# Optimization experiments

Measured on AMD Instinct MI355X. Metric: run time of the kernel, lower is better.

The kernel has to match this reference:

```python
import jax, jax.numpy as jnp
import numpy as np

C = 256

def setup_inputs() -> dict:
    key = jax.random.key(0)
    k1, k2, k3 = jax.random.split(key, 3)
    U = jax.random.normal(k1, (16, C, 128, 128), dtype=jnp.float32)
    # Conv2d 1x1 no-bias weights; kaiming-ish scale
    w_sq = jax.random.normal(k2, (C // 2, C), dtype=jnp.float32) * (1.0 / np.sqrt(C))
    w_ex = jax.random.normal(k3, (C, C // 2), dtype=jnp.float32) * (1.0 / np.sqrt(C // 2))
    return {"U": U, "w_sq": w_sq, "w_ex": w_ex}

def reference(U, w_sq, w_ex):
    # U: [B, C, H, W]
    z = jnp.mean(U, axis=(2, 3))                      # [B, C] global avg pool
    z = jnp.einsum('oc,bc->bo', w_sq, z)              # squeeze: [B, C/2]
    z = jax.nn.relu(z)
    z = jnp.einsum('oc,bc->bo', w_ex, z)              # excite: [B, C]
    s = jax.nn.sigmoid(z)                             # [B, C]
    return U * s[:, :, None, None]                    # broadcast gate over H, W
```

## Files before the change

### kernel.cpp

```cpp
#include <hip/hip_runtime.h>

#define SE_C   256
#define SE_B   16
#define SE_HW  16384

typedef float fx4 __attribute__((ext_vector_type(4)));

__global__ __launch_bounds__(256) void se_pool(const float* __restrict__ U,
                                               float* __restrict__ z) {
    const int plane = blockIdx.x;
    const fx4* Up = (const fx4*)(U + (size_t)plane * SE_HW);
    const int t = threadIdx.x;

    float sum = 0.f;
    #pragma unroll
    for (int k = 0; k < 16; ++k) {
        fx4 v = Up[t + k * 256];
        sum += (v.x + v.y) + (v.z + v.w);
    }
    #pragma unroll
    for (int off = 32; off > 0; off >>= 1)
        sum += __shfl_down(sum, off, 64);

    __shared__ float wsum[4];
    const int lane = t & 63, wid = t >> 6;
    if (lane == 0) wsum[wid] = sum;
    __syncthreads();
    if (t == 0) {
        float tot = (wsum[0] + wsum[1]) + (wsum[2] + wsum[3]);
        z[plane] = tot * (1.0f / SE_HW);
    }
}

__global__ __launch_bounds__(256) void se_fc(const float* __restrict__ z,
                                             const float* __restrict__ w_sq,
                                             const float* __restrict__ w_ex,
                                             float* __restrict__ s) {
    const int b = blockIdx.x;
    const int t = threadIdx.x;

    __shared__ float zb[SE_C];
    __shared__ float h[SE_C / 2];

    zb[t] = z[b * SE_C + t];
    __syncthreads();

    if (t < SE_C / 2) {
        const float* wr = w_sq + t * SE_C;
        float acc = 0.f;
        #pragma unroll 8
        for (int c = 0; c < SE_C; ++c) acc = fmaf(wr[c], zb[c], acc);
        h[t] = fmaxf(acc, 0.f);
    }
    __syncthreads();

    {
        const float* wr = w_ex + t * (SE_C / 2);
        float acc = 0.f;
        #pragma unroll 8
        for (int c = 0; c < SE_C / 2; ++c) acc = fmaf(wr[c], h[c], acc);
        s[b * SE_C + t] = 1.0f / (1.0f + expf(-acc));
    }
}

__global__ __launch_bounds__(256) void se_scale(const float* __restrict__ U,
                                                const float* __restrict__ s,
                                                float* __restrict__ out) {
    const int plane = blockIdx.x;
    const float g = s[plane];
    const fx4* Up = (const fx4*)(U + (size_t)plane * SE_HW);
    fx4* Op = (fx4*)(out + (size_t)plane * SE_HW);
    const int t = threadIdx.x;

    #pragma unroll
    for (int k = 0; k < 16; ++k) {
        fx4 v = Up[t + k * 256];
        v *= g;
        __builtin_nontemporal_store(v, Op + t + k * 256);
    }
}

extern "C" void kernel_launch(void* const* d_in, const int* in_sizes, int n_in,
                              void* d_out, int out_size, void* d_ws, size_t ws_size,
                              hipStream_t stream) {
    const float* U    = (const float*)d_in[0];
    const float* w_sq = (const float*)d_in[1];
    const float* w_ex = (const float*)d_in[2];
    float* out = (float*)d_out;

    float* z = (float*)d_ws;
    float* s = z + SE_B * SE_C;

    se_pool<<<SE_B * SE_C, 256, 0, stream>>>(U, z);
    se_fc<<<SE_B, 256, 0, stream>>>(z, w_sq, w_ex, s);
    se_scale<<<SE_B * SE_C, 256, 0, stream>>>(U, s, out);
}
```

Before: 135.8 us.

## Fuse SE fully-connected gate computation into scale kernel with U prefetch

```diff
diff --git a/kernel.cpp b/kernel.cpp
--- a/kernel.cpp
+++ b/kernel.cpp
@@ -32,12 +32,22 @@
     }
 }
 
-__global__ __launch_bounds__(256) void se_fc(const float* __restrict__ z,
-                                             const float* __restrict__ w_sq,
-                                             const float* __restrict__ w_ex,
-                                             float* __restrict__ s) {
-    const int b = blockIdx.x;
+__global__ __launch_bounds__(256) void se_scale_fc(const float* __restrict__ U,
+                                                   const float* __restrict__ z,
+                                                   const float* __restrict__ w_sq,
+                                                   const float* __restrict__ w_ex,
+                                                   float* __restrict__ out) {
+    const int plane = blockIdx.x;
+    const int b = plane >> 8;
+    const int c = plane & 255;
     const int t = threadIdx.x;
+
+    const fx4* Up = (const fx4*)(U + (size_t)plane * SE_HW);
+    fx4* Op = (fx4*)(out + (size_t)plane * SE_HW);
+
+    fx4 pre[8];
+    #pragma unroll
+    for (int k = 0; k < 8; ++k) pre[k] = Up[t + k * 256];
 
     __shared__ float zb[SE_C];
     __shared__ float h[SE_C / 2];
@@ -49,33 +59,25 @@
         const float* wr = w_sq + t * SE_C;
         float acc = 0.f;
         #pragma unroll 8
-        for (int c = 0; c < SE_C; ++c) acc = fmaf(wr[c], zb[c], acc);
+        for (int k = 0; k < SE_C; ++k) acc = fmaf(wr[k], zb[k], acc);
         h[t] = fmaxf(acc, 0.f);
     }
     __syncthreads();
 
-    {
-        const float* wr = w_ex + t * (SE_C / 2);
-        float acc = 0.f;
-        #pragma unroll 8
-        for (int c = 0; c < SE_C / 2; ++c) acc = fmaf(wr[c], h[c], acc);
-        s[b * SE_C + t] = 1.0f / (1.0f + expf(-acc));
-    }
-}
-
-__global__ __launch_bounds__(256) void se_scale(const float* __restrict__ U,
-                                                const float* __restrict__ s,
-                                                float* __restrict__ out) {
-    const int plane = blockIdx.x;
-    const float g = s[plane];
-    const fx4* Up = (const fx4*)(U + (size_t)plane * SE_HW);
-    fx4* Op = (fx4*)(out + (size_t)plane * SE_HW);
-    const int t = threadIdx.x;
+    const float* we = w_ex + c * (SE_C / 2);
+    float acc = 0.f;
+    #pragma unroll 8
+    for (int k = 0; k < SE_C / 2; ++k) acc = fmaf(we[k], h[k], acc);
+    const float g = 1.0f / (1.0f + __expf(-acc));
 
     #pragma unroll
-    for (int k = 0; k < 16; ++k) {
-        fx4 v = Up[t + k * 256];
-        v *= g;
+    for (int k = 0; k < 8; ++k) {
+        fx4 v = pre[k] * g;
+        __builtin_nontemporal_store(v, Op + t + k * 256);
+    }
+    #pragma unroll
+    for (int k = 8; k < 16; ++k) {
+        fx4 v = Up[t + k * 256] * g;
         __builtin_nontemporal_store(v, Op + t + k * 256);
     }
 }
@@ -89,9 +91,7 @@
     float* out = (float*)d_out;
 
     float* z = (float*)d_ws;
-    float* s = z + SE_B * SE_C;
 
     se_pool<<<SE_B * SE_C, 256, 0, stream>>>(U, z);
-    se_fc<<<SE_B, 256, 0, stream>>>(z, w_sq, w_ex, s);
-    se_scale<<<SE_B * SE_C, 256, 0, stream>>>(U, s, out);
+    se_scale_fc<<<SE_B * SE_C, 256, 0, stream>>>(U, z, w_sq, w_ex, out);
 }
```

New measurement: 164.1 us. 1.21x slower.

## Fuse FC into pooling via last-block counter and chunk batch for cache reuse

Applied to the files above, without the earlier changes.

```diff
diff --git a/kernel.cpp b/kernel.cpp
--- a/kernel.cpp
+++ b/kernel.cpp
@@ -1,17 +1,27 @@
 #include <hip/hip_runtime.h>
 
-#define SE_C   256
-#define SE_B   16
-#define SE_HW  16384
+#define SE_C    256
+#define SE_B    16
+#define SE_HW   16384
+#define CHUNK_B 4
+#define NCHUNK  (SE_B / CHUNK_B)
 
 typedef float fx4 __attribute__((ext_vector_type(4)));
 
-__global__ __launch_bounds__(256) void se_pool(const float* __restrict__ U,
-                                               float* __restrict__ z) {
-    const int plane = blockIdx.x;
-    const fx4* Up = (const fx4*)(U + (size_t)plane * SE_HW);
+__global__ __launch_bounds__(256) void se_pool_fc(const float* __restrict__ U,
+                                                  const float* __restrict__ w_sq,
+                                                  const float* __restrict__ w_ex,
+                                                  float* __restrict__ z,
+                                                  float* __restrict__ s,
+                                                  unsigned* __restrict__ cnt,
+                                                  int b0) {
+    const int local = blockIdx.x;
+    const int b = b0 + (local >> 8);
+    const int c = local & 255;
     const int t = threadIdx.x;
+    const size_t plane = (size_t)b * SE_C + c;
 
+    const fx4* Up = (const fx4*)(U + plane * SE_HW);
     float sum = 0.f;
     #pragma unroll
     for (int k = 0; k < 16; ++k) {
@@ -19,63 +29,59 @@
         sum += (v.x + v.y) + (v.z + v.w);
     }
     #pragma unroll
-    for (int off = 32; off > 0; off >>= 1)
-        sum += __shfl_down(sum, off, 64);
+    for (int off = 32; off > 0; off >>= 1) sum += __shfl_down(sum, off, 64);
 
     __shared__ float wsum[4];
+    __shared__ int isLast;
     const int lane = t & 63, wid = t >> 6;
     if (lane == 0) wsum[wid] = sum;
     __syncthreads();
     if (t == 0) {
         float tot = (wsum[0] + wsum[1]) + (wsum[2] + wsum[3]);
-        z[plane] = tot * (1.0f / SE_HW);
+        __hip_atomic_store(&z[plane], tot * (1.0f / SE_HW),
+                           __ATOMIC_RELEASE, __HIP_MEMORY_SCOPE_AGENT);
+        unsigned prev = __hip_atomic_fetch_add(&cnt[b], 1u,
+                           __ATOMIC_ACQ_REL, __HIP_MEMORY_SCOPE_AGENT);
+        isLast = (prev == SE_C - 1);
     }
-}
-
-__global__ __launch_bounds__(256) void se_fc(const float* __restrict__ z,
-                                             const float* __restrict__ w_sq,
-                                             const float* __restrict__ w_ex,
-                                             float* __restrict__ s) {
-    const int b = blockIdx.x;
-    const int t = threadIdx.x;
+    __syncthreads();
+    if (!isLast) return;
 
     __shared__ float zb[SE_C];
     __shared__ float h[SE_C / 2];
-
-    zb[t] = z[b * SE_C + t];
+    zb[t] = __hip_atomic_load(&z[(size_t)b * SE_C + t],
+                              __ATOMIC_ACQUIRE, __HIP_MEMORY_SCOPE_AGENT);
     __syncthreads();
-
     if (t < SE_C / 2) {
         const float* wr = w_sq + t * SE_C;
         float acc = 0.f;
         #pragma unroll 8
-        for (int c = 0; c < SE_C; ++c) acc = fmaf(wr[c], zb[c], acc);
+        for (int k = 0; k < SE_C; ++k) acc = fmaf(wr[k], zb[k], acc);
         h[t] = fmaxf(acc, 0.f);
     }
     __syncthreads();
-
     {
         const float* wr = w_ex + t * (SE_C / 2);
         float acc = 0.f;
         #pragma unroll 8
-        for (int c = 0; c < SE_C / 2; ++c) acc = fmaf(wr[c], h[c], acc);
-        s[b * SE_C + t] = 1.0f / (1.0f + expf(-acc));
+        for (int k = 0; k < SE_C / 2; ++k) acc = fmaf(wr[k], h[k], acc);
+        s[(size_t)b * SE_C + t] = 1.0f / (1.0f + expf(-acc));
     }
 }
 
 __global__ __launch_bounds__(256) void se_scale(const float* __restrict__ U,
                                                 const float* __restrict__ s,
-                                                float* __restrict__ out) {
-    const int plane = blockIdx.x;
+                                                float* __restrict__ out,
+                                                int b0) {
+    const size_t plane = (size_t)b0 * SE_C + blockIdx.x;
     const float g = s[plane];
-    const fx4* Up = (const fx4*)(U + (size_t)plane * SE_HW);
-    fx4* Op = (fx4*)(out + (size_t)plane * SE_HW);
+    const fx4* Up = (const fx4*)(U + plane * SE_HW);
+    fx4* Op = (fx4*)(out + plane * SE_HW);
     const int t = threadIdx.x;
 
     #pragma unroll
     for (int k = 0; k < 16; ++k) {
-        fx4 v = Up[t + k * 256];
-        v *= g;
+        fx4 v = Up[t + k * 256] * g;
         __builtin_nontemporal_store(v, Op + t + k * 256);
     }
 }
@@ -88,10 +94,15 @@
     const float* w_ex = (const float*)d_in[2];
     float* out = (float*)d_out;
 
-    float* z = (float*)d_ws;
-    float* s = z + SE_B * SE_C;
+    float*    z   = (float*)d_ws;
+    float*    s   = z + SE_B * SE_C;
+    unsigned* cnt = (unsigned*)(s + SE_B * SE_C);
 
-    se_pool<<<SE_B * SE_C, 256, 0, stream>>>(U, z);
-    se_fc<<<SE_B, 256, 0, stream>>>(z, w_sq, w_ex, s);
-    se_scale<<<SE_B * SE_C, 256, 0, stream>>>(U, s, out);
+    hipMemsetAsync(cnt, 0, SE_B * sizeof(unsigned), stream);
+
+    for (int c = 0; c < NCHUNK; ++c) {
+        const int b0 = c * CHUNK_B;
+        se_pool_fc<<<CHUNK_B * SE_C, 256, 0, stream>>>(U, w_sq, w_ex, z, s, cnt, b0);
+        se_scale  <<<CHUNK_B * SE_C, 256, 0, stream>>>(U, s, out, b0);
+    }
 }
```

New measurement: 418.1 us. 3.08x slower.
